# Kernel optimization log

Hardware: AMD Instinct MI355X
Metric: run time of the kernel (lower is better)

Reference implementation:

```python
import jax, jax.numpy as jnp
import numpy as np

N_NODES = 50000
N_EDGES = 1600000
N_FEAT = 256
HIDDEN = 32
N_CLASS = 64
PROP_RANGE = 4
ALPHA = 0.5
BETA = 1.0


def _spmm(edge_src, edge_dst, edge_val, X):
    # sparse propMatrix @ X : gather source rows, scale by edge weight, scatter-add to dst
    msgs = X[edge_src] * edge_val[:, None]            # [E, C]
    return jax.ops.segment_sum(msgs, edge_dst, num_segments=N_NODES)  # [N, C]


def setup_inputs() -> dict:
    key = jax.random.key(0)
    ks = jax.random.split(key, 8)
    x = jax.random.normal(ks[0], (N_NODES, N_FEAT), dtype=jnp.float32)
    edge_src = jax.random.randint(ks[1], (N_EDGES,), 0, N_NODES, dtype=jnp.int32)
    edge_dst = jax.random.randint(ks[2], (N_EDGES,), 0, N_NODES, dtype=jnp.int32)
    edge_val = jax.random.uniform(ks[3], (N_EDGES,), dtype=jnp.float32)
    # predSeq params: Linear(nFeature,32) -> ReLU -> Linear(32,nClass)
    W1 = jax.random.normal(ks[4], (N_FEAT, HIDDEN), dtype=jnp.float32) / np.sqrt(N_FEAT)
    b1 = jnp.zeros((HIDDEN,), dtype=jnp.float32)
    W2 = jax.random.normal(ks[5], (HIDDEN, N_CLASS), dtype=jnp.float32) / np.sqrt(HIDDEN)
    b2 = jnp.zeros((N_CLASS,), dtype=jnp.float32)
    return {"x": x, "edge_src": edge_src, "edge_dst": edge_dst, "edge_val": edge_val,
            "W1": W1, "b1": b1, "W2": W2, "b2": b2}


def reference(x, edge_src, edge_dst, edge_val, W1, b1, W2, b2):
    # predSeq + softmax -> initial pseudo labels [N, nClass]
    h = jax.nn.relu(x @ W1 + b1)
    p = jax.nn.softmax(h @ W2 + b2, axis=1)
    # prop(), mode='none': propRange steps of nonlinear SpMM (dropout = identity in eval)
    for _ in range(PROP_RANGE):
        p = ALPHA * jnp.tanh(BETA * _spmm(edge_src, edge_dst, edge_val, p))
    return jax.nn.softmax(p, axis=1)
```

## Files before the change

### kernel.cpp

```cpp
#include <hip/hip_runtime.h>
#include <hip/hip_bf16.h>
#include <math.h>

#define N_NODES 50000
#define N_EDGES 1600000
#define N_FEAT  256
#define HIDDEN  32
#define N_CLASS 64
#define NBUCK   391
#define EPB     2560
#define BINB    625
#define MLPB    782
#define SCAP    5120
#define CAP     4608

typedef _Float16 half_t;
typedef _Float16 half8 __attribute__((ext_vector_type(8)));

__device__ __forceinline__ float half_tanh(float x) {
  float e = __expf(2.f * x);
  return 0.5f - __builtin_amdgcn_rcpf(e + 1.f);
}


__global__ __launch_bounds__(256) void prep_kernel(
    const float* __restrict__ x, const float* __restrict__ W1,
    const float* __restrict__ b1, const float* __restrict__ W2,
    const float* __restrict__ b2, half_t* __restrict__ P,
    const int* __restrict__ esrc, const int* __restrict__ edst,
    const float* __restrict__ evl, int* __restrict__ bcur,
    int2* __restrict__ st) {
  __shared__ __align__(16) int smem[6684];
  int t = threadIdx.x;

  if (blockIdx.x >= BINB) {
    float* fs = (float*)smem;
    float* xs = fs;
    float* ps = fs;
    float* hfull = fs + 4416;
    int w = __builtin_amdgcn_readfirstlane(t >> 6);
    int l = t & 63;
    int n0 = (blockIdx.x - BINB) * 64;
    int rowb = t >> 4, c4 = t & 15;
    int f0 = c4 * 4;

    float4 v[4];
#pragma unroll
    for (int p = 0; p < 4; ++p) {
      int row = rowb + 16 * p;
      v[p] = make_float4(0.f, 0.f, 0.f, 0.f);
      if (n0 + row < N_NODES)
        v[p] = *(const float4*)(x + (size_t)(n0 + row) * N_FEAT + f0);
    }

    float h[8];
#pragma unroll
    for (int j = 0; j < 8; ++j) h[j] = 0.f;

    for (int kc = 0; kc < 4; ++kc) {
#pragma unroll
      for (int p = 0; p < 4; ++p) {
        int row = rowb + 16 * p;
        int col = (row + f0) & 63;
        xs[(f0 + 0) * 64 + col] = v[p].x;
        xs[(f0 + 1) * 64 + col] = v[p].y;
        xs[(f0 + 2) * 64 + col] = v[p].z;
        xs[(f0 + 3) * 64 + col] = v[p].w;
      }
      __syncthreads();
      if (kc < 3) {
#pragma unroll
        for (int p = 0; p < 4; ++p) {
          int row = rowb + 16 * p;
          v[p] = make_float4(0.f, 0.f, 0.f, 0.f);
          if (n0 + row < N_NODES)
            v[p] = *(const float4*)(x + (size_t)(n0 + row) * N_FEAT + (kc + 1) * 64 + f0);
        }
      }
#pragma unroll 8
      for (int k = 0; k < 64; ++k) {
        float xk = xs[k * 64 + ((l + (k & 60)) & 63)];
        const float* wr = W1 + (size_t)(kc * 64 + k) * HIDDEN + 8 * w;
#pragma unroll
        for (int j = 0; j < 8; ++j) h[j] = fmaf(xk, wr[j], h[j]);
      }
      __syncthreads();
    }

#pragma unroll
    for (int i = 0; i < 8; ++i)
      hfull[l * 33 + 8 * w + i] = fmaxf(h[i] + b1[8 * w + i], 0.f);
    __syncthreads();

    float pa[16];
#pragma unroll
    for (int c = 0; c < 16; ++c) pa[c] = b2[16 * w + c];
#pragma unroll 4
    for (int kk = 0; kk < 32; ++kk) {
      float hk = hfull[l * 33 + kk];
      const float* w2r = W2 + kk * N_CLASS + 16 * w;
#pragma unroll
      for (int c = 0; c < 16; ++c) pa[c] = fmaf(hk, w2r[c], pa[c]);
    }
#pragma unroll
    for (int c = 0; c < 16; ++c) ps[l * 65 + 16 * w + c] = pa[c];
    __syncthreads();

    {
      int n = t >> 2, ck = (t & 3) * 16;
      float q[16];
      float m = -1e30f;
#pragma unroll
      for (int i = 0; i < 16; ++i) { q[i] = ps[n * 65 + ck + i]; m = fmaxf(m, q[i]); }
      m = fmaxf(m, __shfl_xor(m, 1));
      m = fmaxf(m, __shfl_xor(m, 2));
      float s = 0.f;
#pragma unroll
      for (int i = 0; i < 16; ++i) { q[i] = __expf(q[i] - m); s += q[i]; }
      s += __shfl_xor(s, 1);
      s += __shfl_xor(s, 2);
      float inv = 1.f / s;
      if (n0 + n < N_NODES) {
        half8 o0, o1;
#pragma unroll
        for (int i = 0; i < 8; ++i) {
          o0[i] = (half_t)(q[i] * inv);
          o1[i] = (half_t)(q[8 + i] * inv);
        }
        half_t* op = P + (size_t)(n0 + n) * N_CLASS + ck;
        *(half8*)op = o0;
        *(half8*)(op + 8) = o1;
      }
    }
  } else {
    int2* stage = (int2*)smem;
    int* h      = smem + 5120;
    int* lstart = smem + 5511;
    int* lcur   = smem + 5902;
    int* gbase  = smem + 6293;
    int bb = blockIdx.x;
    for (int i = t; i < NBUCK; i += 256) { h[i] = 0; lcur[i] = 0; }
    __syncthreads();
    int base = bb * EPB;
    int nloc = min(EPB, N_EDGES - base);
    for (int i = t; i < nloc; i += 256) atomicAdd(&h[edst[base + i] >> 7], 1);
    __syncthreads();
    if (t < 64) {
      int loc[7];
      int s0 = 0;
#pragma unroll
      for (int i = 0; i < 7; ++i) {
        int b = t * 7 + i;
        int c = (b < NBUCK) ? h[b] : 0;
        loc[i] = s0; s0 += c;
      }
      int run = s0;
#pragma unroll
      for (int off = 1; off < 64; off <<= 1) {
        int u = __shfl_up(run, off);
        if (t >= off) run += u;
      }
      int excl = run - s0;
#pragma unroll
      for (int i = 0; i < 7; ++i) {
        int b = t * 7 + i;
        if (b < NBUCK) lstart[b] = excl + loc[i];
      }
    }
    __syncthreads();
    for (int i = t; i < NBUCK; i += 256) {
      int c = h[i];
      gbase[i] = c ? atomicAdd(&bcur[i], c) : 0;
    }
    __syncthreads();
    for (int i = t; i < nloc; i += 256) {
      int e = base + i;
      int d = edst[e];
      int b = d >> 7;
      int pos = lstart[b] + atomicAdd(&lcur[b], 1);
      stage[pos] = make_int2((d << 16) | esrc[e], __float_as_int(evl[e]));
    }
    __syncthreads();
    for (int i = t; i < nloc; i += 256) {
      int2 vv = stage[i];
      int b = (int)(((unsigned)vv.x) >> 23);
      int pos = gbase[b] + (i - lstart[b]);
      if (pos < SCAP) st[(size_t)b * SCAP + pos] = vv;
    }
  }
}


__global__ __launch_bounds__(1024) void build_csr(const int* __restrict__ bcur,
                                                  const int2* __restrict__ st,
                                                  int2* __restrict__ rr,
                                                  unsigned* __restrict__ ep4) {
  __shared__ int2 stage[CAP];
  __shared__ int lh[128], lstart[128], lcur[128];
  int b = blockIdx.x, t = threadIdx.x;
  int n = min(min(bcur[b], SCAP), CAP);
  int gb = b * SCAP;
  if (t < 128) { lh[t] = 0; lcur[t] = 0; }
  __syncthreads();
  for (int i = t; i < n; i += 1024) {
    int2 v = st[gb + i];
    stage[i] = v;
    atomicAdd(&lh[(v.x >> 16) & 127], 1);
  }
  __syncthreads();
  if (t < 64) {
    int a0 = lh[2 * t], a1 = lh[2 * t + 1];
    int s0 = a0 + a1;
    int run = s0;
#pragma unroll
    for (int off = 1; off < 64; off <<= 1) {
      int u = __shfl_up(run, off);
      if (t >= off) run += u;
    }
    int excl = run - s0;
    lstart[2 * t] = excl;
    lstart[2 * t + 1] = excl + a0;
  }
  __syncthreads();
  int nodebase = b * 128;
  int nn = min(128, N_NODES - nodebase);
  if (t < nn)
    rr[nodebase + t] = make_int2(gb + lstart[t], gb + lstart[t] + lh[t]);
  for (int i = t; i < n; i += 1024) {
    int2 v = stage[i];
    int d = (v.x >> 16) & 127;
    int pos = lstart[d] + atomicAdd(&lcur[d], 1);
    unsigned uh = (unsigned)__builtin_bit_cast(unsigned short,
                                               (_Float16)__int_as_float(v.y));
    ep4[gb + pos] = (unsigned)(v.x & 0xffff) | (uh << 16);
  }
}


template <int FINAL>
__global__ __launch_bounds__(256) void spmm_kernel(const int2* __restrict__ rr,
                                                   const unsigned* __restrict__ ep4,
                                                   const half_t* __restrict__ pin,
                                                   void* __restrict__ pout_) {
  int tid = threadIdx.x;
  int lane = tid & 63;
  int hf = lane >> 5;
  int sl = lane & 31;
  int g = sl >> 3;
  int s = lane & 7;
  int node = blockIdx.x * 8 + (tid >> 6) * 2 + hf;
  int srcb = hf << 5;
  int2 be = rr[node];
  int beg = be.x, end = be.y;
  int deg = end - beg;
  float acc[8];
#pragma unroll
  for (int i = 0; i < 8; ++i) acc[i] = 0.f;

  unsigned raw0 = (sl < deg) ? ep4[beg + sl] : 0u;
  unsigned raw1 = (sl + 32 < deg) ? ep4[beg + sl + 32] : 0u;

  {
    float vjs[16];
    half8 hvv[16];
#pragma unroll
    for (int jj = 0; jj < 8; ++jj) {
      unsigned wj = (unsigned)__shfl((int)raw0, srcb + g + 4 * jj);
      vjs[jj] = (float)__builtin_bit_cast(_Float16, (unsigned short)(wj >> 16));
      hvv[jj] = *(const half8*)(pin + ((size_t)(wj & 0xffffu) << 6) + (s << 3));
    }
#pragma unroll
    for (int jj = 0; jj < 8; ++jj) {
      unsigned wj = (unsigned)__shfl((int)raw1, srcb + g + 4 * jj);
      vjs[8 + jj] = (float)__builtin_bit_cast(_Float16, (unsigned short)(wj >> 16));
      hvv[8 + jj] = *(const half8*)(pin + ((size_t)(wj & 0xffffu) << 6) + (s << 3));
    }
#pragma unroll
    for (int jj = 0; jj < 16; ++jj)
#pragma unroll
      for (int i = 0; i < 8; ++i)
        acc[i] = fmaf(vjs[jj], (float)hvv[jj][i], acc[i]);
  }
  if (deg > 64) {
    for (int base = beg + 64; base < end; base += 32) {
      int idx = base + sl;
      unsigned raw = (idx < end) ? ep4[idx] : 0u;
      int cnt = min(32, end - base);
#pragma unroll 4
      for (int j = g; j < cnt; j += 4) {
        unsigned wj = (unsigned)__shfl((int)raw, srcb + j);
        float vj = (float)__builtin_bit_cast(_Float16, (unsigned short)(wj >> 16));
        half8 hv = *(const half8*)(pin + ((size_t)(wj & 0xffffu) << 6) + (s << 3));
#pragma unroll
        for (int i = 0; i < 8; ++i) acc[i] = fmaf(vj, (float)hv[i], acc[i]);
      }
    }
  }

#pragma unroll
  for (int off = 8; off <= 16; off <<= 1)
#pragma unroll
    for (int i = 0; i < 8; ++i) acc[i] += __shfl_xor(acc[i], off);
  float r[8];
#pragma unroll
  for (int i = 0; i < 8; ++i) r[i] = half_tanh(acc[i]);
  if (FINAL) {
    float m = r[0];
#pragma unroll
    for (int i = 1; i < 8; ++i) m = fmaxf(m, r[i]);
    m = fmaxf(m, __shfl_xor(m, 1));
    m = fmaxf(m, __shfl_xor(m, 2));
    m = fmaxf(m, __shfl_xor(m, 4));
    float e[8], sum = 0.f;
#pragma unroll
    for (int i = 0; i < 8; ++i) { e[i] = __expf(r[i] - m); sum += e[i]; }
    sum += __shfl_xor(sum, 1);
    sum += __shfl_xor(sum, 2);
    sum += __shfl_xor(sum, 4);
    float inv = 1.f / sum;
    if (g == 0) {
      float* op = (float*)pout_ + ((size_t)node << 6) + (s << 3);
      *(float4*)op = make_float4(e[0] * inv, e[1] * inv, e[2] * inv, e[3] * inv);
      *(float4*)(op + 4) = make_float4(e[4] * inv, e[5] * inv, e[6] * inv, e[7] * inv);
    }
  } else {
    if (g == 0) {
      half8 o;
#pragma unroll
      for (int i = 0; i < 8; ++i) o[i] = (half_t)r[i];
      *(half8*)((half_t*)pout_ + ((size_t)node << 6) + (s << 3)) = o;
    }
  }
}


extern "C" void kernel_launch(void* const* d_in, const int* in_sizes, int n_in,
                              void* d_out, int out_size, void* d_ws, size_t ws_size,
                              hipStream_t stream) {
  const float* x    = (const float*)d_in[0];
  const int*   esrc = (const int*)d_in[1];
  const int*   edst = (const int*)d_in[2];
  const float* evl  = (const float*)d_in[3];
  const float* W1   = (const float*)d_in[4];
  const float* b1   = (const float*)d_in[5];
  const float* W2   = (const float*)d_in[6];
  const float* b2   = (const float*)d_in[7];

  char* ws = (char*)d_ws;
  int2*     st   = (int2*)    (ws);
  half_t*   Pb   = (half_t*)  (ws);
  unsigned* ep4  = (unsigned*)(ws + 16015360);
  half_t*   Pa   = (half_t*)  (ws + 24023040);
  int*      bcur = (int*)     (ws + 30423040);
  int2*     rr   = (int2*)    (ws + 30424640);

  hipMemsetAsync(bcur, 0, NBUCK * sizeof(int), stream);

  prep_kernel<<<MLPB + BINB, 256, 0, stream>>>(x, W1, b1, W2, b2, Pa,
                                               esrc, edst, evl, bcur, st);
  build_csr<<<NBUCK, 1024, 0, stream>>>(bcur, st, rr, ep4);

  spmm_kernel<0><<<6250, 256, 0, stream>>>(rr, ep4, Pa, (void*)Pb);
  spmm_kernel<0><<<6250, 256, 0, stream>>>(rr, ep4, Pb, (void*)Pa);
  spmm_kernel<0><<<6250, 256, 0, stream>>>(rr, ep4, Pa, (void*)Pb);
  spmm_kernel<1><<<6250, 256, 0, stream>>>(rr, ep4, Pb, d_out);
}
```

Measured before the change: 239.2 us.

## Store propagated label matrices in FP8 e4m3 instead of FP16

The intermediate probability matrices passed between SpMM iterations are stored as FP8 e4m3 instead of half precision. This halves the bytes per gathered row. The SpMM lane mapping changes so each lane loads 16 bytes covering 16 classes and eight edges are processed in parallel per half-wave. Accumulation, tanh and the final softmax stay in fp32. The cost is much lower precision on the intermediates, which may exceed the tolerance, plus extra scalar conversion instructions.

```diff
diff --git a/kernel.cpp b/kernel.cpp
--- a/kernel.cpp
+++ b/kernel.cpp
@@ -1,5 +1,6 @@
 #include <hip/hip_runtime.h>
 #include <hip/hip_bf16.h>
+#include <hip/hip_fp8.h>
 #include <math.h>
 
 #define N_NODES 50000
@@ -15,18 +16,35 @@
 #define CAP     4608
 
 typedef _Float16 half_t;
-typedef _Float16 half8 __attribute__((ext_vector_type(8)));
 
 __device__ __forceinline__ float half_tanh(float x) {
   float e = __expf(2.f * x);
   return 0.5f - __builtin_amdgcn_rcpf(e + 1.f);
 }
 
+__device__ __forceinline__ void fp8x4_to_f32(unsigned w, float* f) {
+  unsigned char b0 = w & 0xff, b1 = (w >> 8) & 0xff,
+                b2 = (w >> 16) & 0xff, b3 = (w >> 24) & 0xff;
+  f[0] = (float)(*reinterpret_cast<const __hip_fp8_e4m3*>(&b0));
+  f[1] = (float)(*reinterpret_cast<const __hip_fp8_e4m3*>(&b1));
+  f[2] = (float)(*reinterpret_cast<const __hip_fp8_e4m3*>(&b2));
+  f[3] = (float)(*reinterpret_cast<const __hip_fp8_e4m3*>(&b3));
+}
+__device__ __forceinline__ unsigned f32x4_to_fp8(const float* f) {
+  unsigned r = 0;
+#pragma unroll
+  for (int k = 0; k < 4; ++k) {
+    __hip_fp8_e4m3 t(f[k]);
+    r |= (unsigned)__builtin_bit_cast(unsigned char, t) << (8 * k);
+  }
+  return r;
+}
+
 
 __global__ __launch_bounds__(256) void prep_kernel(
     const float* __restrict__ x, const float* __restrict__ W1,
     const float* __restrict__ b1, const float* __restrict__ W2,
-    const float* __restrict__ b2, half_t* __restrict__ P,
+    const float* __restrict__ b2, unsigned char* __restrict__ P,
     const int* __restrict__ esrc, const int* __restrict__ edst,
     const float* __restrict__ evl, int* __restrict__ bcur,
     int2* __restrict__ st) {
@@ -121,15 +139,12 @@
       s += __shfl_xor(s, 2);
       float inv = 1.f / s;
       if (n0 + n < N_NODES) {
-        half8 o0, o1;
-#pragma unroll
-        for (int i = 0; i < 8; ++i) {
-          o0[i] = (half_t)(q[i] * inv);
-          o1[i] = (half_t)(q[8 + i] * inv);
-        }
-        half_t* op = P + (size_t)(n0 + n) * N_CLASS + ck;
-        *(half8*)op = o0;
-        *(half8*)(op + 8) = o1;
+        float vals[16];
+#pragma unroll
+        for (int i = 0; i < 16; ++i) vals[i] = q[i] * inv;
+        int4 o = make_int4((int)f32x4_to_fp8(vals + 0),  (int)f32x4_to_fp8(vals + 4),
+                           (int)f32x4_to_fp8(vals + 8),  (int)f32x4_to_fp8(vals + 12));
+        *(int4*)(P + (size_t)(n0 + n) * 64 + ck) = o;
       }
     }
   } else {
@@ -240,95 +255,115 @@
 template <int FINAL>
 __global__ __launch_bounds__(256) void spmm_kernel(const int2* __restrict__ rr,
                                                    const unsigned* __restrict__ ep4,
-                                                   const half_t* __restrict__ pin,
+                                                   const unsigned char* __restrict__ pin,
                                                    void* __restrict__ pout_) {
   int tid = threadIdx.x;
   int lane = tid & 63;
   int hf = lane >> 5;
   int sl = lane & 31;
-  int g = sl >> 3;
-  int s = lane & 7;
+  int q = lane & 3;
+  int g = (lane >> 2) & 7;
   int node = blockIdx.x * 8 + (tid >> 6) * 2 + hf;
   int srcb = hf << 5;
   int2 be = rr[node];
   int beg = be.x, end = be.y;
   int deg = end - beg;
-  float acc[8];
-#pragma unroll
-  for (int i = 0; i < 8; ++i) acc[i] = 0.f;
+  float acc[16];
+#pragma unroll
+  for (int i = 0; i < 16; ++i) acc[i] = 0.f;
 
   unsigned raw0 = (sl < deg) ? ep4[beg + sl] : 0u;
   unsigned raw1 = (sl + 32 < deg) ? ep4[beg + sl + 32] : 0u;
 
   {
-    float vjs[16];
-    half8 hvv[16];
+    float vjs[8];
+    int4 hvv[8];
+#pragma unroll
+    for (int jj = 0; jj < 4; ++jj) {
+      unsigned wj = (unsigned)__shfl((int)raw0, srcb + g + 8 * jj);
+      vjs[jj] = (float)__builtin_bit_cast(_Float16, (unsigned short)(wj >> 16));
+      hvv[jj] = *(const int4*)(pin + ((size_t)(wj & 0xffffu) << 6) + (q << 4));
+    }
+#pragma unroll
+    for (int jj = 0; jj < 4; ++jj) {
+      unsigned wj = (unsigned)__shfl((int)raw1, srcb + g + 8 * jj);
+      vjs[4 + jj] = (float)__builtin_bit_cast(_Float16, (unsigned short)(wj >> 16));
+      hvv[4 + jj] = *(const int4*)(pin + ((size_t)(wj & 0xffffu) << 6) + (q << 4));
+    }
 #pragma unroll
     for (int jj = 0; jj < 8; ++jj) {
-      unsigned wj = (unsigned)__shfl((int)raw0, srcb + g + 4 * jj);
-      vjs[jj] = (float)__builtin_bit_cast(_Float16, (unsigned short)(wj >> 16));
-      hvv[jj] = *(const half8*)(pin + ((size_t)(wj & 0xffffu) << 6) + (s << 3));
-    }
-#pragma unroll
-    for (int jj = 0; jj < 8; ++jj) {
-      unsigned wj = (unsigned)__shfl((int)raw1, srcb + g + 4 * jj);
-      vjs[8 + jj] = (float)__builtin_bit_cast(_Float16, (unsigned short)(wj >> 16));
-      hvv[8 + jj] = *(const half8*)(pin + ((size_t)(wj & 0xffffu) << 6) + (s << 3));
-    }
-#pragma unroll
-    for (int jj = 0; jj < 16; ++jj)
-#pragma unroll
-      for (int i = 0; i < 8; ++i)
-        acc[i] = fmaf(vjs[jj], (float)hvv[jj][i], acc[i]);
+      float f[4];
+      fp8x4_to_f32((unsigned)hvv[jj].x, f);
+#pragma unroll
+      for (int k = 0; k < 4; ++k) acc[k] = fmaf(vjs[jj], f[k], acc[k]);
+      fp8x4_to_f32((unsigned)hvv[jj].y, f);
+#pragma unroll
+      for (int k = 0; k < 4; ++k) acc[4 + k] = fmaf(vjs[jj], f[k], acc[4 + k]);
+      fp8x4_to_f32((unsigned)hvv[jj].z, f);
+#pragma unroll
+      for (int k = 0; k < 4; ++k) acc[8 + k] = fmaf(vjs[jj], f[k], acc[8 + k]);
+      fp8x4_to_f32((unsigned)hvv[jj].w, f);
+#pragma unroll
+      for (int k = 0; k < 4; ++k) acc[12 + k] = fmaf(vjs[jj], f[k], acc[12 + k]);
+    }
   }
   if (deg > 64) {
     for (int base = beg + 64; base < end; base += 32) {
       int idx = base + sl;
       unsigned raw = (idx < end) ? ep4[idx] : 0u;
       int cnt = min(32, end - base);
-#pragma unroll 4
-      for (int j = g; j < cnt; j += 4) {
+      for (int j = g; j < cnt; j += 8) {
         unsigned wj = (unsigned)__shfl((int)raw, srcb + j);
         float vj = (float)__builtin_bit_cast(_Float16, (unsigned short)(wj >> 16));
-        half8 hv = *(const half8*)(pin + ((size_t)(wj & 0xffffu) << 6) + (s << 3));
-#pragma unroll
-        for (int i = 0; i < 8; ++i) acc[i] = fmaf(vj, (float)hv[i], acc[i]);
-      }
-    }
-  }
-
-#pragma unroll
-  for (int off = 8; off <= 16; off <<= 1)
-#pragma unroll
-    for (int i = 0; i < 8; ++i) acc[i] += __shfl_xor(acc[i], off);
-  float r[8];
-#pragma unroll
-  for (int i = 0; i < 8; ++i) r[i] = half_tanh(acc[i]);
+        int4 hv = *(const int4*)(pin + ((size_t)(wj & 0xffffu) << 6) + (q << 4));
+        float f[4];
+        fp8x4_to_f32((unsigned)hv.x, f);
+#pragma unroll
+        for (int k = 0; k < 4; ++k) acc[k] = fmaf(vj, f[k], acc[k]);
+        fp8x4_to_f32((unsigned)hv.y, f);
+#pragma unroll
+        for (int k = 0; k < 4; ++k) acc[4 + k] = fmaf(vj, f[k], acc[4 + k]);
+        fp8x4_to_f32((unsigned)hv.z, f);
+#pragma unroll
+        for (int k = 0; k < 4; ++k) acc[8 + k] = fmaf(vj, f[k], acc[8 + k]);
+        fp8x4_to_f32((unsigned)hv.w, f);
+#pragma unroll
+        for (int k = 0; k < 4; ++k) acc[12 + k] = fmaf(vj, f[k], acc[12 + k]);
+      }
+    }
+  }
+
+#pragma unroll
+  for (int off = 4; off <= 16; off <<= 1)
+#pragma unroll
+    for (int i = 0; i < 16; ++i) acc[i] += __shfl_xor(acc[i], off);
+  float r[16];
+#pragma unroll
+  for (int i = 0; i < 16; ++i) r[i] = half_tanh(acc[i]);
   if (FINAL) {
     float m = r[0];
 #pragma unroll
-    for (int i = 1; i < 8; ++i) m = fmaxf(m, r[i]);
+    for (int i = 1; i < 16; ++i) m = fmaxf(m, r[i]);
     m = fmaxf(m, __shfl_xor(m, 1));
     m = fmaxf(m, __shfl_xor(m, 2));
-    m = fmaxf(m, __shfl_xor(m, 4));
-    float e[8], sum = 0.f;
-#pragma unroll
-    for (int i = 0; i < 8; ++i) { e[i] = __expf(r[i] - m); sum += e[i]; }
+    float e[16], sum = 0.f;
+#pragma unroll
+    for (int i = 0; i < 16; ++i) { e[i] = __expf(r[i] - m); sum += e[i]; }
     sum += __shfl_xor(sum, 1);
     sum += __shfl_xor(sum, 2);
-    sum += __shfl_xor(sum, 4);
     float inv = 1.f / sum;
     if (g == 0) {
-      float* op = (float*)pout_ + ((size_t)node << 6) + (s << 3);
-      *(float4*)op = make_float4(e[0] * inv, e[1] * inv, e[2] * inv, e[3] * inv);
-      *(float4*)(op + 4) = make_float4(e[4] * inv, e[5] * inv, e[6] * inv, e[7] * inv);
+      float* op = (float*)pout_ + ((size_t)node << 6) + (q << 4);
+      *(float4*)(op + 0)  = make_float4(e[0] * inv,  e[1] * inv,  e[2] * inv,  e[3] * inv);
+      *(float4*)(op + 4)  = make_float4(e[4] * inv,  e[5] * inv,  e[6] * inv,  e[7] * inv);
+      *(float4*)(op + 8)  = make_float4(e[8] * inv,  e[9] * inv,  e[10] * inv, e[11] * inv);
+      *(float4*)(op + 12) = make_float4(e[12] * inv, e[13] * inv, e[14] * inv, e[15] * inv);
     }
   } else {
     if (g == 0) {
-      half8 o;
-#pragma unroll
-      for (int i = 0; i < 8; ++i) o[i] = (half_t)r[i];
-      *(half8*)((half_t*)pout_ + ((size_t)node << 6) + (s << 3)) = o;
+      int4 o = make_int4((int)f32x4_to_fp8(r + 0),  (int)f32x4_to_fp8(r + 4),
+                         (int)f32x4_to_fp8(r + 8),  (int)f32x4_to_fp8(r + 12));
+      *(int4*)((unsigned char*)pout_ + ((size_t)node << 6) + (q << 4)) = o;
     }
   }
 }
@@ -347,12 +382,12 @@
   const float* b2   = (const float*)d_in[7];
 
   char* ws = (char*)d_ws;
-  int2*     st   = (int2*)    (ws);
-  half_t*   Pb   = (half_t*)  (ws);
-  unsigned* ep4  = (unsigned*)(ws + 16015360);
-  half_t*   Pa   = (half_t*)  (ws + 24023040);
-  int*      bcur = (int*)     (ws + 30423040);
-  int2*     rr   = (int2*)    (ws + 30424640);
+  int2*          st   = (int2*)     (ws);
+  unsigned char* Pb   = (unsigned char*)(ws);
+  unsigned*      ep4  = (unsigned*) (ws + 16015360);
+  unsigned char* Pa   = (unsigned char*)(ws + 24023040);
+  int*           bcur = (int*)      (ws + 27223040);
+  int2*          rr   = (int2*)     (ws + 27224640);
 
   hipMemsetAsync(bcur, 0, NBUCK * sizeof(int), stream);
 
```

New measurement: 271.2 us. 13.4% more time.
